# Kernel optimization log

Hardware: AMD Instinct MI355X
Metric: run time of the kernel (lower is better)

## Reference

```python
import jax, jax.numpy as jnp
import numpy as np

N_GAUSSIANS = 512
N_PIXELS = 262144  # 512x512 image


def setup_inputs() -> dict:
    key = jax.random.key(0)
    k1, k2, k3, k4, k5 = jax.random.split(key, 5)
    x = jax.random.uniform(k1, (N_PIXELS, 2), dtype=jnp.float32)
    alphas = (1.0 / N_GAUSSIANS) ** 0.5 * jax.random.uniform(k2, (N_GAUSSIANS, 1), dtype=jnp.float32)
    means = jax.random.uniform(k3, (N_GAUSSIANS, 2), dtype=jnp.float32)
    rotations = jnp.pi * jax.random.uniform(k4, (N_GAUSSIANS, 1), dtype=jnp.float32)
    scales = 0.1 * jax.random.uniform(k5, (N_GAUSSIANS, 2), dtype=jnp.float32)
    return {"x": x, "alphas": alphas, "means": means, "rotations": rotations, "scales": scales}


def _inv2x2(m):
    # m: [N, 2, 2] -> elementwise 2x2 inverse
    a, b = m[:, 0, 0], m[:, 0, 1]
    c, d = m[:, 1, 0], m[:, 1, 1]
    det = a * d - b * c
    inv = jnp.stack([jnp.stack([d, -b], axis=-1),
                     jnp.stack([-c, a], axis=-1)], axis=-2)
    return inv / det[:, None, None]


def reference(x, alphas, means, rotations, scales):
    rot = rotations[:, 0]                       # [N]
    cth, sth = jnp.cos(rot), jnp.sin(rot)
    s0, s1 = scales[:, 0], scales[:, 1]
    # RS = R @ diag(s): [N, 2, 2]
    RS = jnp.stack([s0 * cth, -s1 * sth, s0 * sth, s1 * cth], axis=-1).reshape(-1, 2, 2)
    RSSR = jnp.einsum('nij,nkj->nik', RS, RS)   # RS @ RS^T
    cov = _inv2x2(RSSR)                          # [N, 2, 2]
    rel = x[:, None, :] - means[None, :, :]      # [P, N, 2]
    q = jnp.einsum('pni,nij,pnj->pn', rel, cov, rel)  # quadratic form [P, N]
    g = jnp.exp(-q / 2)                          # [P, N]
    return g @ alphas                            # [P, 1]
```

## Files before the change

kernel.cpp:

```cpp
#include <hip/hip_runtime.h>

#define NG 512
#define NPX 262144
#define BLOCK 256
#define GTILE 8

#if __has_builtin(__builtin_amdgcn_exp2f)
  #define KSCALE 0.72134752044448170368f
  #define EXPNEG(w) __builtin_amdgcn_exp2f(-(w))
#else
  #define KSCALE 0.5f
  #define EXPNEG(w) __expf(-(w))
#endif

__global__ void gsplat_prep(const float* __restrict__ alphas,
                            const float* __restrict__ means,
                            const float* __restrict__ rotations,
                            const float* __restrict__ scales,
                            float4* __restrict__ ga,
                            float2* __restrict__ gb)
{
    int n = blockIdx.x * blockDim.x + threadIdx.x;
    if (n >= NG) return;

    float rot = rotations[n];
    float sth, cth;
    sincosf(rot, &sth, &cth);
    float s0 = scales[2 * n + 0];
    float s1 = scales[2 * n + 1];
    float r00 = s0 * cth, r01 = -s1 * sth;
    float r10 = s0 * sth, r11 =  s1 * cth;
    float Ar = r00 * r00 + r01 * r01;
    float Br = r00 * r10 + r01 * r11;
    float Dr = r10 * r10 + r11 * r11;
    float det = Ar * Dr - Br * Br;
    float kc00 =  KSCALE * Dr / det;
    float kc01 = -KSCALE * Br / det;
    float p00 = sqrtf(kc00);
    float p01 = kc01 / p00;
    float p11 = sqrtf(KSCALE / Dr);
    float mx = means[2 * n + 0];
    float my = means[2 * n + 1];
    float nuoff = -(p00 * mx + p01 * my);
    float nvoff = -(p11 * my);

    ga[n] = make_float4(p00, p01, nuoff, alphas[n]);
    gb[n] = make_float2(p11, nvoff);
}

__global__ __launch_bounds__(BLOCK)
void gsplat_main(const float* __restrict__ x,
                 const float4* __restrict__ ga,
                 const float2* __restrict__ gb,
                 float* __restrict__ out)
{
    int tid = blockIdx.x * BLOCK + threadIdx.x;
    float2 xv = ((const float2*)x)[tid];
    float x0 = xv.x, y0 = xv.y;

    float acc0 = 0.0f, acc1 = 0.0f;
    for (int t = 0; t < NG; t += GTILE) {
        float4 a[GTILE];
        float2 b[GTILE];
        #pragma unroll
        for (int j = 0; j < GTILE; ++j) {
            a[j] = ga[t + j];
            b[j] = gb[t + j];
        }
        #pragma unroll
        for (int j = 0; j < GTILE; ++j) {
            float u = fmaf(a[j].x, x0, fmaf(a[j].y, y0, a[j].z));
            float v = fmaf(b[j].x, y0, b[j].y);
            float w = fmaf(v, v, u * u);
            float e = EXPNEG(w);
            if (j & 1) acc1 = fmaf(a[j].w, e, acc1);
            else       acc0 = fmaf(a[j].w, e, acc0);
        }
    }

    out[tid] = acc0 + acc1;
}

extern "C" void kernel_launch(void* const* d_in, const int* in_sizes, int n_in,
                              void* d_out, int out_size, void* d_ws, size_t ws_size,
                              hipStream_t stream) {
    const float* x         = (const float*)d_in[0];
    const float* alphas    = (const float*)d_in[1];
    const float* means     = (const float*)d_in[2];
    const float* rotations = (const float*)d_in[3];
    const float* scales    = (const float*)d_in[4];
    float* out = (float*)d_out;

    float4* ga = (float4*)d_ws;
    float2* gb = (float2*)((char*)d_ws + NG * 16);

    gsplat_prep<<<(NG + 255) / 256, 256, 0, stream>>>(alphas, means, rotations, scales, ga, gb);

    int grid = NPX / BLOCK;
    gsplat_main<<<grid, BLOCK, 0, stream>>>(x, ga, gb, out);
}
```

Measured before the change: 96.40 us.

## Process two pixels per thread with double-buffered gaussian parameter loads

Each thread now evaluates two pixels (one from each half of the image), so every gaussian parameter load is reused across two pixels. The per-gaussian loads are software-pipelined with a ping-pong register buffer, fetching the next tile of four while the current tile is computed. The grid is halved, which lowers the number of waves in flight and raises register use per thread; the exp throughput remains the main limit.

```diff
diff --git a/kernel.cpp b/kernel.cpp
--- a/kernel.cpp
+++ b/kernel.cpp
@@ -3,7 +3,9 @@
 #define NG 512
 #define NPX 262144
 #define BLOCK 256
-#define GTILE 8
+#define GTILE 4
+#define PPT 2
+#define HALFPX (NPX / 2)
 
 #if __has_builtin(__builtin_amdgcn_exp2f)
   #define KSCALE 0.72134752044448170368f
@@ -55,30 +57,58 @@
                  float* __restrict__ out)
 {
     int tid = blockIdx.x * BLOCK + threadIdx.x;
-    float2 xv = ((const float2*)x)[tid];
-    float x0 = xv.x, y0 = xv.y;
+    float2 pv0 = ((const float2*)x)[tid];
+    float2 pv1 = ((const float2*)x)[tid + HALFPX];
+    float x0 = pv0.x, y0 = pv0.y;
+    float x1 = pv1.x, y1 = pv1.y;
 
-    float acc0 = 0.0f, acc1 = 0.0f;
-    for (int t = 0; t < NG; t += GTILE) {
-        float4 a[GTILE];
-        float2 b[GTILE];
+    float accA0 = 0.0f, accA1 = 0.0f;
+    float accB0 = 0.0f, accB1 = 0.0f;
+
+    float4 ca[GTILE]; float2 cb[GTILE];
+    float4 na[GTILE]; float2 nb[GTILE];
+
+    #pragma unroll
+    for (int j = 0; j < GTILE; ++j) { ca[j] = ga[j]; cb[j] = gb[j]; }
+
+    #define COMPUTE_TILE(A, B)                                                \
+        _Pragma("unroll")                                                     \
+        for (int j = 0; j < GTILE; ++j) {                                     \
+            float czu = A[j].z;              \
+            float czv = B[j].y;                                               \
+            float u0 = fmaf(A[j].x, x0, fmaf(A[j].y, y0, czu));               \
+            float v0 = fmaf(B[j].x, y0, czv);                                 \
+            float w0 = fmaf(v0, v0, u0 * u0);                                 \
+            float e0 = EXPNEG(w0);                                            \
+            float u1 = fmaf(A[j].x, x1, fmaf(A[j].y, y1, czu));               \
+            float v1 = fmaf(B[j].x, y1, czv);                                 \
+            float w1 = fmaf(v1, v1, u1 * u1);                                 \
+            float e1 = EXPNEG(w1);                                            \
+            if (j & 1) { accA1 = fmaf(A[j].w, e0, accA1);                     \
+                         accB1 = fmaf(A[j].w, e1, accB1); }                   \
+            else       { accA0 = fmaf(A[j].w, e0, accA0);                     \
+                         accB0 = fmaf(A[j].w, e1, accB0); }                   \
+        }
+
+    for (int t = 0; t < NG; t += 2 * GTILE) {
         #pragma unroll
         for (int j = 0; j < GTILE; ++j) {
-            a[j] = ga[t + j];
-            b[j] = gb[t + j];
+            int n = (t + GTILE + j) & (NG - 1);
+            na[j] = ga[n]; nb[j] = gb[n];
         }
+        COMPUTE_TILE(ca, cb)
+
         #pragma unroll
         for (int j = 0; j < GTILE; ++j) {
-            float u = fmaf(a[j].x, x0, fmaf(a[j].y, y0, a[j].z));
-            float v = fmaf(b[j].x, y0, b[j].y);
-            float w = fmaf(v, v, u * u);
-            float e = EXPNEG(w);
-            if (j & 1) acc1 = fmaf(a[j].w, e, acc1);
-            else       acc0 = fmaf(a[j].w, e, acc0);
+            int n = (t + 2 * GTILE + j) & (NG - 1);
+            ca[j] = ga[n]; cb[j] = gb[n];
         }
+        COMPUTE_TILE(na, nb)
     }
+    #undef COMPUTE_TILE
 
-    out[tid] = acc0 + acc1;
+    out[tid]          = accA0 + accA1;
+    out[tid + HALFPX] = accB0 + accB1;
 }
 
 extern "C" void kernel_launch(void* const* d_in, const int* in_sizes, int n_in,
@@ -96,6 +126,6 @@
 
     gsplat_prep<<<(NG + 255) / 256, 256, 0, stream>>>(alphas, means, rotations, scales, ga, gb);
 
-    int grid = NPX / BLOCK;
+    int grid = NPX / (BLOCK * PPT);
     gsplat_main<<<grid, BLOCK, 0, stream>>>(x, ga, gb, out);
 }
```

Result: slower. 99.63 us (+3.3%).
